# Optimization experiments

Hardware: AMD Instinct MI355X
Metric: run time of the kernel (lower is better)

## Reference

```python
import jax, jax.numpy as jnp
import numpy as np

NUM_HEADS = 15
NUM_KV_HEADS = 5
HEAD_DIM = 64
GROUPS = NUM_HEADS // NUM_KV_HEADS
BIG_NEG = jnp.finfo(jnp.float32).min


def setup_inputs() -> dict:
    key = jax.random.key(0)
    k1, k2, k3, k4 = jax.random.split(key, 4)
    B, S = 2, 2048
    attention_mask = jax.random.randint(k1, (B, S, S), 0, 2).astype(bool)
    query_states = jax.random.normal(k2, (B, S, NUM_HEADS, HEAD_DIM), dtype=jnp.float32)
    key_states = jax.random.normal(k3, (B, S, NUM_KV_HEADS, HEAD_DIM), dtype=jnp.float32)
    value_states = jax.random.normal(k4, (B, S, NUM_KV_HEADS, HEAD_DIM), dtype=jnp.float32)
    return {
        "attention_mask": attention_mask,
        "query_states": query_states,
        "key_states": key_states,
        "value_states": value_states,
    }


def reference(attention_mask, query_states, key_states, value_states):
    B, S = query_states.shape[0], key_states.shape[1]
    # GQA: expand KV heads (each kv head repeated GROUPS times, contiguous)
    k = jnp.repeat(key_states, GROUPS, axis=2)    # [B,S,H,D]
    v = jnp.repeat(value_states, GROUPS, axis=2)  # [B,S,H,D]
    q = query_states.astype(jnp.float32)
    k = k.astype(jnp.float32)
    # scores: [B,H,Sq,Sk]
    att = jnp.einsum('bqhd,bkhd->bhqk', q, k) * (HEAD_DIM ** -0.5)
    maskf = attention_mask[:, None, :, :].astype(jnp.float32)
    att = maskf * att + (1.0 - maskf) * BIG_NEG
    probs = jax.nn.softmax(att, axis=-1).astype(v.dtype)
    # [B,H,Sq,D] -> [B,Sq,H,D] -> [B,Sq,H*D]
    out = jnp.einsum('bhqk,bkhd->bqhd', probs, v)
    return out.reshape(B, S, NUM_HEADS * HEAD_DIM)
```

## Files before the change

### kernel.cpp

```cpp
#include <hip/hip_runtime.h>
#include <hip/hip_bf16.h>

#define B_    2
#define S_    2048
#define H_    15
#define KVH_  5
#define G_    3
#define D_    64
#define KVD_  (KVH_ * D_)
#define HD_   (H_ * D_)
#define SW_   (S_ / 32)
#define KBLK  32
#define ITER  (S_ / KBLK)

constexpr float SCALE   = 0.125f;
constexpr float NEG_BIG = -3.0e38f;
constexpr float DEFER_THR = 8.0f;

typedef __bf16  bf16x8 __attribute__((ext_vector_type(8)));
typedef __bf16  bf16x4 __attribute__((ext_vector_type(4)));
typedef float   f32x4  __attribute__((ext_vector_type(4)));
typedef int     i32x4  __attribute__((ext_vector_type(4)));

#define MFMA(a, b, c) __builtin_amdgcn_mfma_f32_16x16x32_bf16((a), (b), (c), 0, 0, 0)

__device__ __forceinline__ void gload16(const void* g, void* l) {
    __builtin_amdgcn_global_load_lds(
        (const __attribute__((address_space(1))) unsigned int*)g,
        (__attribute__((address_space(3))) unsigned int*)l, 16, 0, 0);
}

__device__ __forceinline__ unsigned pack_hi16(unsigned even_elem, unsigned odd_elem) {
    return __builtin_amdgcn_perm(odd_elem, even_elem, 0x07060302u);
}

__global__ __launch_bounds__(256) void bitpack(const int* __restrict__ mask,
                                               unsigned int* __restrict__ bits) {
    const int i = blockIdx.x * 256 + threadIdx.x;
    unsigned long long bal = __ballot(mask[i] != 0);
    const int lane = threadIdx.x & 63;
    if (lane == 0)       bits[i >> 5] = (unsigned int)bal;
    else if (lane == 32) bits[i >> 5] = (unsigned int)(bal >> 32);
}

__global__ __launch_bounds__(256) void conv_k(const float* __restrict__ K,
                                              __bf16* __restrict__ khi,
                                              __bf16* __restrict__ klo) {
    const int i = blockIdx.x * 256 + threadIdx.x;
    const float4 v = ((const float4*)K)[i];
    const float xs[4] = {v.x, v.y, v.z, v.w};
    bf16x4 h, lo;
#pragma unroll
    for (int j = 0; j < 4; j++) {
        __bf16 hh = (__bf16)xs[j];
        h[j]  = hh;
        lo[j] = (__bf16)(xs[j] - (float)hh);
    }
    ((bf16x4*)khi)[i] = h;
    ((bf16x4*)klo)[i] = lo;
}

__global__ __launch_bounds__(256) void transpose_v(const float* __restrict__ V,
                                                   __bf16* __restrict__ vthi,
                                                   __bf16* __restrict__ vtlo) {
    __shared__ float tile[64][65];
    const int bid = blockIdx.x;
    const int st  = bid & 31;
    const int kv  = (bid >> 5) % KVH_;
    const int b   = bid / (32 * KVH_);
    const int s0  = st * 64;
    const int tid = threadIdx.x;
    const int c   = tid & 63;
    const int rq  = tid >> 6;
#pragma unroll
    for (int i = 0; i < 16; i++) {
        const int si = rq + i * 4;
        tile[si][c] = V[(((size_t)b * S_ + s0 + si) * KVH_ + kv) * D_ + c];
    }
    __syncthreads();
#pragma unroll
    for (int i = 0; i < 16; i++) {
        const int di = rq + i * 4;
        const float x = tile[c][di];
        const __bf16 hh = (__bf16)x;
        const size_t o = (((size_t)b * KVH_ + kv) * D_ + di) * S_ + s0 + c;
        vthi[o] = hh;
        vtlo[o] = (__bf16)(x - (float)hh);
    }
}

__global__ __launch_bounds__(256) void attn_main(const unsigned int* __restrict__ bits,
                                                 const float* __restrict__ Q,
                                                 const __bf16* __restrict__ khi,
                                                 const __bf16* __restrict__ klo,
                                                 const __bf16* __restrict__ vthi,
                                                 const __bf16* __restrict__ vtlo,
                                                 float* __restrict__ out) {
    __shared__ __align__(16) __bf16   Kls[2][2][KBLK][64];
    __shared__ __align__(16) __bf16   Vls[2][64][KBLK];
    __shared__ __align__(16) unsigned Pw[4][2][16][20];

    const int tid  = threadIdx.x;
    const int wv   = tid >> 6;
    const int lane = tid & 63;
    const int lrow = lane & 15;
    const int lgrp = lane >> 4;

    const int bid = blockIdx.x;
    const int qt  = bid & 31;
    const int bh  = bid >> 5;
    const int h   = bh % H_;
    const int b   = bh / H_;
    const int kv  = h / G_;
    const int q0  = qt * 64 + wv * 16;

    const float* qp = Q + (((size_t)b * S_ + (q0 + lrow)) * H_ + h) * D_;
    bf16x8 ahi[2], alo[2];
#pragma unroll
    for (int kk = 0; kk < 2; kk++) {
#pragma unroll
        for (int jj = 0; jj < 2; jj++) {
            const float4 v = *(const float4*)(qp + kk * 32 + lgrp * 8 + jj * 4);
            const float xs[4] = {v.x * SCALE, v.y * SCALE, v.z * SCALE, v.w * SCALE};
#pragma unroll
            for (int j = 0; j < 4; j++) {
                const __bf16 hh = (__bf16)xs[j];
                ahi[kk][jj * 4 + j] = hh;
                alo[kk][jj * 4 + j] = (__bf16)(xs[j] - (float)hh);
            }
        }
    }

    f32x4 O[4] = {{0.f,0.f,0.f,0.f},{0.f,0.f,0.f,0.f},{0.f,0.f,0.f,0.f},{0.f,0.f,0.f,0.f}};
    float m = NEG_BIG, l = 0.f;

    const __bf16* khb = khi + (size_t)b * S_ * KVD_ + kv * D_;
    const __bf16* klb = klo + (size_t)b * S_ * KVD_ + kv * D_;
    const __bf16* vhb = vthi + ((size_t)b * KVH_ + kv) * D_ * S_;
    const __bf16* vlb = vtlo + ((size_t)b * KVH_ + kv) * D_ * S_;

    const int kgi  = wv * 64 + lane;
    const int krow = kgi >> 3, kcg = kgi & 7;
    const int kcol = ((kcg ^ (krow & 7)) * 8);
    const int vrow = kgi >> 2, vcg = kgi & 3;
    const int vcol = ((vcg ^ ((vrow >> 1) & 3)) * 8);

    const __bf16* khsrc = khb + (size_t)krow * KVD_ + kcol;
    const __bf16* klsrc = klb + (size_t)krow * KVD_ + kcol;
    const __bf16* vhsrc = vhb + (size_t)vrow * S_ + vcol;
    const __bf16* vlsrc = vlb + (size_t)vrow * S_ + vcol;
    const unsigned int* bptr = bits + ((size_t)b * S_ + q0 + lrow) * SW_;

    gload16(khsrc, &Kls[0][0][wv * 8][0]);
    gload16(klsrc, &Kls[0][1][wv * 8][0]);
    khsrc += (size_t)KBLK * KVD_;
    klsrc += (size_t)KBLK * KVD_;
    __syncthreads();

    for (int kt = 0; kt < ITER; kt++) {
        const int cur = kt & 1;

        const unsigned w = *bptr++;

        if (kt + 1 < ITER) {
            gload16(khsrc, &Kls[cur ^ 1][0][wv * 8][0]);
            gload16(klsrc, &Kls[cur ^ 1][1][wv * 8][0]);
            khsrc += (size_t)KBLK * KVD_;
            klsrc += (size_t)KBLK * KVD_;
        }
        gload16(vhsrc, &Vls[0][wv * 16][0]);
        gload16(vlsrc, &Vls[1][wv * 16][0]);
        vhsrc += KBLK;
        vlsrc += KBLK;

        f32x4 s[2];
#pragma unroll
        for (int t = 0; t < 2; t++) {
            const int row = t * 16 + lrow;
            const int sw  = row & 7;
            const bf16x8 bh0 = *(const bf16x8*)&Kls[cur][0][row][(lgrp ^ sw) * 8];
            const bf16x8 bh1 = *(const bf16x8*)&Kls[cur][0][row][((4 + lgrp) ^ sw) * 8];
            const bf16x8 bl0 = *(const bf16x8*)&Kls[cur][1][row][(lgrp ^ sw) * 8];
            const bf16x8 bl1 = *(const bf16x8*)&Kls[cur][1][row][((4 + lgrp) ^ sw) * 8];
            f32x4 acc = {0.f, 0.f, 0.f, 0.f};
            acc = MFMA(bh0, ahi[0], acc);
            acc = MFMA(bh0, alo[0], acc);
            acc = MFMA(bl0, ahi[0], acc);
            acc = MFMA(bh1, ahi[1], acc);
            acc = MFMA(bh1, alo[1], acc);
            acc = MFMA(bl1, ahi[1], acc);
            s[t] = acc;
        }

        float pmax = NEG_BIG;
#pragma unroll
        for (int t = 0; t < 2; t++) {
#pragma unroll
            for (int r = 0; r < 4; r++) {
                const int bit = t * 16 + lgrp * 4 + r;
                const float sv = ((w >> bit) & 1u) ? s[t][r] : NEG_BIG;
                s[t][r] = sv;
                pmax = fmaxf(pmax, sv);
            }
        }
        pmax = fmaxf(pmax, __shfl_xor(pmax, 16));
        pmax = fmaxf(pmax, __shfl_xor(pmax, 32));

        if (!__all(pmax <= m + DEFER_THR)) {
            const float mn = fmaxf(m, pmax);
            const float f  = __expf(m - mn);
            m = mn;
            l *= f;
#pragma unroll
            for (int db = 0; db < 4; db++) {
                f32x4 o = O[db];
                o[0] *= f; o[1] *= f; o[2] *= f; o[3] *= f;
                O[db] = o;
            }
        }

#pragma unroll
        for (int t = 0; t < 2; t++) {
            unsigned words[2][2];
#pragma unroll
            for (int pr = 0; pr < 2; pr++) {
                const float e0 = __expf(s[t][2 * pr]     - m);
                const float e1 = __expf(s[t][2 * pr + 1] - m);
                l += e0 + e1;
                const unsigned u0 = __builtin_bit_cast(unsigned, e0);
                const unsigned u1 = __builtin_bit_cast(unsigned, e1);
                const float h0 = __builtin_bit_cast(float, u0 & 0xFFFF0000u);
                const float h1 = __builtin_bit_cast(float, u1 & 0xFFFF0000u);
                const unsigned l0 = __builtin_bit_cast(unsigned, e0 - h0);
                const unsigned l1 = __builtin_bit_cast(unsigned, e1 - h1);
                words[0][pr] = pack_hi16(u0, u1);
                words[1][pr] = pack_hi16(l0, l1);
            }
            *(uint2*)&Pw[wv][0][lrow][8 * t + 2 * lgrp] = make_uint2(words[0][0], words[0][1]);
            *(uint2*)&Pw[wv][1][lrow][8 * t + 2 * lgrp] = make_uint2(words[1][0], words[1][1]);
        }
        __syncthreads();

        const bf16x8 ph = __builtin_bit_cast(bf16x8, *(const i32x4*)&Pw[wv][0][lrow][lgrp * 4]);
        const bf16x8 pl = __builtin_bit_cast(bf16x8, *(const i32x4*)&Pw[wv][1][lrow][lgrp * 4]);
#pragma unroll
        for (int db = 0; db < 4; db++) {
            const int row = db * 16 + lrow;
            const int sw  = (row >> 1) & 3;
            const bf16x8 vh = *(const bf16x8*)&Vls[0][row][(lgrp ^ sw) * 8];
            const bf16x8 vl = *(const bf16x8*)&Vls[1][row][(lgrp ^ sw) * 8];
            O[db] = MFMA(vh, ph, O[db]);
            O[db] = MFMA(vh, pl, O[db]);
            O[db] = MFMA(vl, ph, O[db]);
        }
        __syncthreads();
    }

    float lv = l;
    lv += __shfl_xor(lv, 16);
    lv += __shfl_xor(lv, 32);
    const float inv = 1.0f / lv;
    float* op = out + ((size_t)b * S_ + q0 + lrow) * HD_ + h * D_ + lgrp * 4;
#pragma unroll
    for (int db = 0; db < 4; db++) {
        f32x4 o = O[db];
        o[0] *= inv; o[1] *= inv; o[2] *= inv; o[3] *= inv;
        *(f32x4*)(op + db * 16) = o;
    }
}

extern "C" void kernel_launch(void* const* d_in, const int* in_sizes, int n_in,
                              void* d_out, int out_size, void* d_ws, size_t ws_size,
                              hipStream_t stream) {
    const int*   mask = (const int*)d_in[0];
    const float* Q    = (const float*)d_in[1];
    const float* K    = (const float*)d_in[2];
    const float* V    = (const float*)d_in[3];
    float*       out  = (float*)d_out;

    char* ws = (char*)d_ws;
    unsigned int* bits = (unsigned int*)ws;
    const size_t KV_BYTES = (size_t)B_ * S_ * KVH_ * D_ * sizeof(__bf16);
    __bf16* khi  = (__bf16*)(ws + (1 << 20));
    __bf16* klo  = (__bf16*)(ws + (1 << 20) + KV_BYTES);
    __bf16* vthi = (__bf16*)(ws + (1 << 20) + 2 * KV_BYTES);
    __bf16* vtlo = (__bf16*)(ws + (1 << 20) + 3 * KV_BYTES);

    bitpack<<<(B_ * S_ * S_) / 256, 256, 0, stream>>>(mask, bits);
    conv_k<<<(B_ * S_ * KVH_ * D_) / (256 * 4), 256, 0, stream>>>(K, khi, klo);
    transpose_v<<<B_ * KVH_ * (S_ / 64), 256, 0, stream>>>(V, vthi, vtlo);
    attn_main<<<B_ * H_ * (S_ / 64), 256, 0, stream>>>(bits, Q, khi, klo, vthi, vtlo, out);
}
```

Baseline: 245.5 us.

## Permute K rows so P stays in registers; double-buffer V; grid-stride bitpack

K rows are loaded in a permuted key order so each lane's QK^T accumulator values already match the B-operand layout needed by the PV MFMA. The P values can then be packed directly in registers, removing the LDS staging buffer and one __syncthreads per iteration. The mask bit index is remapped to match the permutation. V tiles are now double-buffered alongside K, the bitpack kernel uses a grid-stride loop over 2048 blocks, and transpose_v runs with 512 threads. The risk is a mismatch between the key permutation and the mask bit mapping, which would give wrong results.

```diff
diff --git a/kernel.cpp b/kernel.cpp
--- a/kernel.cpp
+++ b/kernel.cpp
@@ -36,11 +36,13 @@
 
 __global__ __launch_bounds__(256) void bitpack(const int* __restrict__ mask,
                                                unsigned int* __restrict__ bits) {
-    const int i = blockIdx.x * 256 + threadIdx.x;
-    unsigned long long bal = __ballot(mask[i] != 0);
-    const int lane = threadIdx.x & 63;
-    if (lane == 0)       bits[i >> 5] = (unsigned int)bal;
-    else if (lane == 32) bits[i >> 5] = (unsigned int)(bal >> 32);
+    const int stride = gridDim.x * 256;
+    const int lane   = threadIdx.x & 63;
+    for (int i = blockIdx.x * 256 + threadIdx.x; i < B_ * S_ * S_; i += stride) {
+        unsigned long long bal = __ballot(mask[i] != 0);
+        if (lane == 0)       bits[i >> 5] = (unsigned int)bal;
+        else if (lane == 32) bits[i >> 5] = (unsigned int)(bal >> 32);
+    }
 }
 
 __global__ __launch_bounds__(256) void conv_k(const float* __restrict__ K,
@@ -60,7 +62,7 @@
     ((bf16x4*)klo)[i] = lo;
 }
 
-__global__ __launch_bounds__(256) void transpose_v(const float* __restrict__ V,
+__global__ __launch_bounds__(512) void transpose_v(const float* __restrict__ V,
                                                    __bf16* __restrict__ vthi,
                                                    __bf16* __restrict__ vtlo) {
     __shared__ float tile[64][65];
@@ -73,14 +75,14 @@
     const int c   = tid & 63;
     const int rq  = tid >> 6;
 #pragma unroll
-    for (int i = 0; i < 16; i++) {
-        const int si = rq + i * 4;
+    for (int i = 0; i < 8; i++) {
+        const int si = rq + i * 8;
         tile[si][c] = V[(((size_t)b * S_ + s0 + si) * KVH_ + kv) * D_ + c];
     }
     __syncthreads();
 #pragma unroll
-    for (int i = 0; i < 16; i++) {
-        const int di = rq + i * 4;
+    for (int i = 0; i < 8; i++) {
+        const int di = rq + i * 8;
         const float x = tile[c][di];
         const __bf16 hh = (__bf16)x;
         const size_t o = (((size_t)b * KVH_ + kv) * D_ + di) * S_ + s0 + c;
@@ -96,9 +98,8 @@
                                                  const __bf16* __restrict__ vthi,
                                                  const __bf16* __restrict__ vtlo,
                                                  float* __restrict__ out) {
-    __shared__ __align__(16) __bf16   Kls[2][2][KBLK][64];
-    __shared__ __align__(16) __bf16   Vls[2][64][KBLK];
-    __shared__ __align__(16) unsigned Pw[4][2][16][20];
+    __shared__ __align__(16) __bf16 Kls[2][2][KBLK][64];
+    __shared__ __align__(16) __bf16 Vls[2][2][64][KBLK];
 
     const int tid  = threadIdx.x;
     const int wv   = tid >> 6;
@@ -140,21 +141,26 @@
     const __bf16* vlb = vtlo + ((size_t)b * KVH_ + kv) * D_ * S_;
 
     const int kgi  = wv * 64 + lane;
-    const int krow = kgi >> 3, kcg = kgi & 7;
-    const int kcol = ((kcg ^ (krow & 7)) * 8);
+    const int krho = kgi >> 3;
+    const int kkey = 8 * ((krho >> 2) & 3) + 4 * (krho >> 4) + (krho & 3);
+    const int kcol = (((kgi & 7) ^ (krho & 7)) * 8);
     const int vrow = kgi >> 2, vcg = kgi & 3;
     const int vcol = ((vcg ^ ((vrow >> 1) & 3)) * 8);
 
-    const __bf16* khsrc = khb + (size_t)krow * KVD_ + kcol;
-    const __bf16* klsrc = klb + (size_t)krow * KVD_ + kcol;
+    const __bf16* khsrc = khb + (size_t)kkey * KVD_ + kcol;
+    const __bf16* klsrc = klb + (size_t)kkey * KVD_ + kcol;
     const __bf16* vhsrc = vhb + (size_t)vrow * S_ + vcol;
     const __bf16* vlsrc = vlb + (size_t)vrow * S_ + vcol;
     const unsigned int* bptr = bits + ((size_t)b * S_ + q0 + lrow) * SW_;
 
     gload16(khsrc, &Kls[0][0][wv * 8][0]);
     gload16(klsrc, &Kls[0][1][wv * 8][0]);
+    gload16(vhsrc, &Vls[0][0][wv * 16][0]);
+    gload16(vlsrc, &Vls[0][1][wv * 16][0]);
     khsrc += (size_t)KBLK * KVD_;
     klsrc += (size_t)KBLK * KVD_;
+    vhsrc += KBLK;
+    vlsrc += KBLK;
     __syncthreads();
 
     for (int kt = 0; kt < ITER; kt++) {
@@ -165,13 +171,13 @@
         if (kt + 1 < ITER) {
             gload16(khsrc, &Kls[cur ^ 1][0][wv * 8][0]);
             gload16(klsrc, &Kls[cur ^ 1][1][wv * 8][0]);
+            gload16(vhsrc, &Vls[cur ^ 1][0][wv * 16][0]);
+            gload16(vlsrc, &Vls[cur ^ 1][1][wv * 16][0]);
             khsrc += (size_t)KBLK * KVD_;
             klsrc += (size_t)KBLK * KVD_;
-        }
-        gload16(vhsrc, &Vls[0][wv * 16][0]);
-        gload16(vlsrc, &Vls[1][wv * 16][0]);
-        vhsrc += KBLK;
-        vlsrc += KBLK;
+            vhsrc += KBLK;
+            vlsrc += KBLK;
+        }
 
         f32x4 s[2];
 #pragma unroll
@@ -197,7 +203,7 @@
         for (int t = 0; t < 2; t++) {
 #pragma unroll
             for (int r = 0; r < 4; r++) {
-                const int bit = t * 16 + lgrp * 4 + r;
+                const int bit = 8 * lgrp + 4 * t + r;
                 const float sv = ((w >> bit) & 1u) ? s[t][r] : NEG_BIG;
                 s[t][r] = sv;
                 pmax = fmaxf(pmax, sv);
@@ -219,9 +225,9 @@
             }
         }
 
+        unsigned hw[4], lw[4];
 #pragma unroll
         for (int t = 0; t < 2; t++) {
-            unsigned words[2][2];
 #pragma unroll
             for (int pr = 0; pr < 2; pr++) {
                 const float e0 = __expf(s[t][2 * pr]     - m);
@@ -233,26 +239,27 @@
                 const float h1 = __builtin_bit_cast(float, u1 & 0xFFFF0000u);
                 const unsigned l0 = __builtin_bit_cast(unsigned, e0 - h0);
                 const unsigned l1 = __builtin_bit_cast(unsigned, e1 - h1);
-                words[0][pr] = pack_hi16(u0, u1);
-                words[1][pr] = pack_hi16(l0, l1);
+                hw[2 * t + pr] = pack_hi16(u0, u1);
+                lw[2 * t + pr] = pack_hi16(l0, l1);
             }
-            *(uint2*)&Pw[wv][0][lrow][8 * t + 2 * lgrp] = make_uint2(words[0][0], words[0][1]);
-            *(uint2*)&Pw[wv][1][lrow][8 * t + 2 * lgrp] = make_uint2(words[1][0], words[1][1]);
-        }
-        __syncthreads();
-
-        const bf16x8 ph = __builtin_bit_cast(bf16x8, *(const i32x4*)&Pw[wv][0][lrow][lgrp * 4]);
-        const bf16x8 pl = __builtin_bit_cast(bf16x8, *(const i32x4*)&Pw[wv][1][lrow][lgrp * 4]);
+        }
+        i32x4 wh, wl;
+#pragma unroll
+        for (int i = 0; i < 4; i++) { wh[i] = (int)hw[i]; wl[i] = (int)lw[i]; }
+        const bf16x8 ph = __builtin_bit_cast(bf16x8, wh);
+        const bf16x8 pl = __builtin_bit_cast(bf16x8, wl);
+
 #pragma unroll
         for (int db = 0; db < 4; db++) {
             const int row = db * 16 + lrow;
             const int sw  = (row >> 1) & 3;
-            const bf16x8 vh = *(const bf16x8*)&Vls[0][row][(lgrp ^ sw) * 8];
-            const bf16x8 vl = *(const bf16x8*)&Vls[1][row][(lgrp ^ sw) * 8];
+            const bf16x8 vh = *(const bf16x8*)&Vls[cur][0][row][(lgrp ^ sw) * 8];
+            const bf16x8 vl = *(const bf16x8*)&Vls[cur][1][row][(lgrp ^ sw) * 8];
             O[db] = MFMA(vh, ph, O[db]);
             O[db] = MFMA(vh, pl, O[db]);
             O[db] = MFMA(vl, ph, O[db]);
         }
+
         __syncthreads();
     }
 
@@ -286,8 +293,8 @@
     __bf16* vthi = (__bf16*)(ws + (1 << 20) + 2 * KV_BYTES);
     __bf16* vtlo = (__bf16*)(ws + (1 << 20) + 3 * KV_BYTES);
 
-    bitpack<<<(B_ * S_ * S_) / 256, 256, 0, stream>>>(mask, bits);
+    bitpack<<<2048, 256, 0, stream>>>(mask, bits);
     conv_k<<<(B_ * S_ * KVH_ * D_) / (256 * 4), 256, 0, stream>>>(K, khi, klo);
-    transpose_v<<<B_ * KVH_ * (S_ / 64), 256, 0, stream>>>(V, vthi, vtlo);
+    transpose_v<<<B_ * KVH_ * (S_ / 64), 512, 0, stream>>>(V, vthi, vtlo);
     attn_main<<<B_ * H_ * (S_ / 64), 256, 0, stream>>>(bits, Q, khi, klo, vthi, vtlo, out);
 }
```

New measurement: 232.4 us. -5.3%, faster.
